# Performance work log

Hardware: AMD Instinct MI355X
Metric: run time of the kernel (lower is better)

Reference implementation:

```python
import jax, jax.numpy as jnp
import numpy as np

N, CIN, T, V, COUT = 64, 64, 256, 25, 128
CI = COUT // 2  # inter_channels
EPS = 1e-5


def setup_inputs() -> dict:
    key = jax.random.key(0)
    ks = jax.random.split(key, 12)
    s = 0.05
    d = {}
    d['x'] = jax.random.normal(ks[0], (N, CIN, T, V), jnp.float32)
    d['A'] = jax.random.normal(ks[1], (3, V, V), jnp.float32) * s
    d['Al'] = jax.random.normal(ks[2], (3, V, V), jnp.float32) * s
    d['Wp'] = jax.random.normal(ks[3], (3, COUT, CIN), jnp.float32) * s
    d['bp'] = jnp.zeros((3, COUT), jnp.float32)
    d['Wm1'] = jax.random.normal(ks[4], (CI, CIN), jnp.float32) * s
    d['bm1'] = jnp.zeros((CI,), jnp.float32)
    d['Wm2'] = jax.random.normal(ks[5], (CI, CIN), jnp.float32) * s
    d['bm2'] = jnp.zeros((CI,), jnp.float32)
    d['Wm3'] = jax.random.normal(ks[6], (COUT, CI), jnp.float32) * s
    d['bm3'] = jnp.zeros((COUT,), jnp.float32)
    d['Wm4'] = jax.random.normal(ks[7], (COUT, CIN), jnp.float32) * s
    d['bm4'] = jnp.zeros((COUT,), jnp.float32)
    d['alpha'] = jax.random.normal(ks[8], (1,), jnp.float32) * s
    d['bn_gamma'] = jnp.ones((COUT,), jnp.float32)
    d['bn_beta'] = jnp.zeros((COUT,), jnp.float32)
    d['down_W'] = jax.random.normal(ks[9], (COUT, CIN), jnp.float32) * s
    d['down_gamma'] = jnp.ones((COUT,), jnp.float32)
    d['down_beta'] = jnp.zeros((COUT,), jnp.float32)
    return d


def _bn_train(y, gamma, beta):
    # BatchNorm2d training forward: biased batch stats over (N, T, V)
    mu = jnp.mean(y, axis=(0, 2, 3), keepdims=True)
    var = jnp.var(y, axis=(0, 2, 3), keepdims=True)
    return (y - mu) * jax.lax.rsqrt(var + EPS) * gamma[None, :, None, None] + beta[None, :, None, None]


def reference(x, A, Al, Wp, bp, Wm1, bm1, Wm2, bm2, Wm3, bm3, Wm4, bm4,
              alpha, bn_gamma, bn_beta, down_W, down_gamma, down_beta):
    Tn = x.shape[2]
    # --- static graph branch: sum over 3 subsets of (A+Al) graph matmuls ---
    Xp = jnp.einsum('soi,nitv->snotv', Wp, x) + bp[:, None, :, None, None]  # (3,N,COUT,T,V)
    y = jnp.einsum('suv,snctv->nctu', A + Al, Xp)                           # (N,COUT,T,V)
    # --- dynamic adjacency from temporal-difference features ---
    xf = jnp.mean(jnp.einsum('oi,nitv->notv', Wm1, x[:, :, :Tn - 2]) + bm1[None, :, None, None], axis=2)  # (N,CI,V)
    xb = jnp.mean(jnp.einsum('oi,nitv->notv', Wm2, x[:, :, 2:]) + bm2[None, :, None, None], axis=2)       # (N,CI,V)
    diff = xb[:, :, :, None] - xf[:, :, None, :]                            # (N,CI,V,V)
    Rd = jnp.tanh(jnp.einsum('oi,nivw->novw', Wm3, diff) + bm3[None, :, None, None])  # (N,COUT,V,V)
    Xm = jnp.einsum('oi,nitv->notv', Wm4, x) + bm4[None, :, None, None]     # (N,COUT,T,V)
    z = jnp.einsum('ncuv,nctv->nctu', Rd, Xm)                               # (N,COUT,T,V)
    y = z * alpha + y
    # --- BN, residual (1x1 conv + BN down-path since CIN != COUT), ReLU ---
    y = _bn_train(y, bn_gamma, bn_beta)
    d = jnp.einsum('oi,nitv->notv', down_W, x)  # no bias
    d = _bn_train(d, down_gamma, down_beta)
    return jax.nn.relu(y + d)
```

## Files before the change

### kernel.cpp

```cpp
#include <hip/hip_runtime.h>
#include <stdint.h>

typedef unsigned short u16;
typedef unsigned int   u32;
typedef short bf16x8 __attribute__((ext_vector_type(8)));
typedef float f32x4  __attribute__((ext_vector_type(4)));

#define N_    64
#define CIN_  64
#define T_    256
#define V_    25
#define COUT_ 128
#define CI_   64
#define EPS_  1e-5f
#define CNT_  409600.0f

#define MFMA16(a,b,c) __builtin_amdgcn_mfma_f32_16x16x32_bf16((a),(b),(c),0,0,0)

__device__ __forceinline__ u16 f2bf(float f) {
  u32 u = __float_as_uint(f);
  u += 0x7fffu + ((u >> 16) & 1u);
  return (u16)(u >> 16);
}
__device__ __forceinline__ float bf2f(u16 h) { return __uint_as_float(((u32)h) << 16); }

__global__ __launch_bounds__(256) void k_pack(const float* __restrict__ Wp, const float* __restrict__ Wm4,
                                              const float* __restrict__ dW, const float* __restrict__ A,
                                              const float* __restrict__ Al,
                                              u16* __restrict__ w5, u16* __restrict__ bst,
                                              float* __restrict__ rsumw) {
  int tid = threadIdx.x;
  for (int i = tid; i < 640 * 64; i += 256) {
    int r = i >> 6, k = i & 63;
    float v = (r < 384) ? Wp[i] : (r < 512) ? Wm4[(r - 384) * 64 + k] : dW[(r - 512) * 64 + k];
    w5[i] = f2bf(v);
  }
  for (int i = tid; i < 3 * 32 * 32; i += 256) {
    int s = i >> 10, rem = i & 1023, u = rem >> 5, v = rem & 31;
    float val = (u < 25 && v < 25) ? (A[(s * 25 + u) * 25 + v] + Al[(s * 25 + u) * 25 + v]) : 0.f;
    bst[i] = f2bf(val);
  }
  if (tid < 75) {
    int s = tid / 25, u = tid % 25;
    float acc = 0.f;
    for (int v = 0; v < 25; v++) acc += A[(s * 25 + u) * 25 + v] + Al[(s * 25 + u) * 25 + v];
    rsumw[tid] = acc;
  }
}

__global__ __launch_bounds__(256) void k_means(const float* __restrict__ x,
                                               float* __restrict__ mf, float* __restrict__ mb) {
  int i = blockIdx.x, n = blockIdx.y;
  const float* src = x + ((size_t)n * CIN_ + i) * T_ * V_;
  __shared__ float xs[T_ * V_];
  __shared__ float pf[8][32], pb[8][32];
  {
    float4* xs4 = (float4*)xs;
    const float4* src4 = (const float4*)src;
    for (int idx = threadIdx.x; idx < (T_ * V_) / 4; idx += 256) xs4[idx] = src4[idx];
  }
  __syncthreads();
  int v = threadIdx.x & 31, g = threadIdx.x >> 5;
  float sf = 0.f, sb = 0.f;
  if (v < V_) {
    for (int t = g; t < T_; t += 8) {
      float val = xs[t * V_ + v];
      if (t < T_ - 2) sf += val;
      if (t >= 2)     sb += val;
    }
  }
  pf[g][v] = sf; pb[g][v] = sb;
  __syncthreads();
  if (threadIdx.x < V_) {
    float af = 0.f, ab = 0.f;
    for (int gg = 0; gg < 8; gg++) { af += pf[gg][threadIdx.x]; ab += pb[gg][threadIdx.x]; }
    size_t o = ((size_t)n * CIN_ + i) * V_ + threadIdx.x;
    mf[o] = af * (1.0f / 254.0f);
    mb[o] = ab * (1.0f / 254.0f);
  }
}

__global__ __launch_bounds__(256) void k_rd1(
    const float* __restrict__ mf, const float* __restrict__ mb,
    const float* __restrict__ Wm1, const float* __restrict__ bm1,
    const float* __restrict__ Wm2, const float* __restrict__ bm2,
    const float* __restrict__ Wm3, float* __restrict__ pqws) {
  int n = blockIdx.x, tid = threadIdx.x;
  __shared__ float MfL[CIN_][V_], MbL[CIN_][V_], xfL[CI_][V_], xbL[CI_][V_];
  for (int idx = tid; idx < CIN_ * V_; idx += 256) {
    MfL[idx / V_][idx % V_] = mf[(size_t)n * CIN_ * V_ + idx];
    MbL[idx / V_][idx % V_] = mb[(size_t)n * CIN_ * V_ + idx];
  }
  __syncthreads();
  for (int idx = tid; idx < CI_ * V_; idx += 256) {
    int o = idx / V_, v = idx % V_;
    float af = bm1[o], ab = bm2[o];
    for (int i = 0; i < CIN_; i++) {
      af += Wm1[o * CIN_ + i] * MfL[i][v];
      ab += Wm2[o * CIN_ + i] * MbL[i][v];
    }
    xfL[o][v] = af; xbL[o][v] = ab;
  }
  __syncthreads();
  for (int idx = tid; idx < COUT_ * V_; idx += 256) {
    int c = idx / V_, u = idx % V_;
    float p = 0.f, q = 0.f;
    for (int i = 0; i < CI_; i++) {
      p += Wm3[c * CI_ + i] * xbL[i][u];
      q += Wm3[c * CI_ + i] * xfL[i][u];
    }
    pqws[(size_t)n * 6400 + idx] = p;
    pqws[(size_t)n * 6400 + 3200 + idx] = q;
  }
}

__global__ __launch_bounds__(256) void k_rd2(
    const float* __restrict__ pqws, const float* __restrict__ rsumw,
    const float* __restrict__ bm3, const float* __restrict__ bm4,
    const float* __restrict__ bp, const float* __restrict__ alpha,
    u16* __restrict__ rdws, float* __restrict__ biasws) {
  int cg = blockIdx.x, n = blockIdx.y;
  int c0 = cg * 16, tid = threadIdx.x;
  __shared__ float Ps[400], Qs[400], rs[75];
  for (int idx = tid; idx < 400; idx += 256) {
    Ps[idx] = pqws[(size_t)n * 6400 + c0 * 25 + idx];
    Qs[idx] = pqws[(size_t)n * 6400 + 3200 + c0 * 25 + idx];
  }
  if (tid < 75) rs[tid] = rsumw[tid];
  __syncthreads();
  float al = alpha[0];
  for (int r = tid; r < 400; r += 256) {
    int cl = r / 25, u = r - cl * 25, c = c0 + cl;
    float pv = Ps[r] + bm3[c];
    float acc = 0.f;
    u16* dst = rdws + ((size_t)(n * COUT_ + c) * 25 + u) * 32;
    for (int w0 = 0; w0 < 25; w0++) {
      float val = al * tanhf(pv - Qs[cl * 25 + w0]);
      dst[w0] = f2bf(val);
      acc += val;
    }
    for (int w0 = 25; w0 < 32; w0++) dst[w0] = 0;
    float yb = 0.f;
    for (int s = 0; s < 3; s++) yb += bp[s * COUT_ + c] * rs[s * 25 + u];
    biasws[(size_t)(n * COUT_ + c) * 25 + u] = bm4[c] * acc + yb;
  }
}

__global__ __launch_bounds__(256, 2) void k_main(
    const float* __restrict__ x, const u16* __restrict__ w5, const u16* __restrict__ bst,
    const u16* __restrict__ rdws, const float* __restrict__ biasws,
    u16* __restrict__ out16, float* __restrict__ partials) {
  __shared__ __align__(16) char smem[36864];
  __shared__ float statsL[512];
  const int tid = threadIdx.x;
  const int w = tid >> 6, l = tid & 63;
  const int lc = l & 15, lq = l >> 4;
  const int n = blockIdx.y, tc = blockIdx.x, t0 = tc * 16;

  bf16x8 bw[3][2];
  #pragma unroll
  for (int s = 0; s < 3; s++)
    #pragma unroll
    for (int ut = 0; ut < 2; ut++)
      bw[s][ut] = *(const bf16x8*)(bst + (s * 32 + ut * 16 + lc) * 32 + lq * 8);

  bf16x8 xf[7][2] = {};
  const float* xb = x + (size_t)n * CIN_ * T_ * V_ + (size_t)t0 * V_;
  #pragma unroll
  for (int ks = 0; ks < 2; ks++) {
    u32* xslw = (u32*)smem;
    for (int idx = tid; idx < 16 * 416; idx += 256) {
      int i2 = idx / 416, p = idx - i2 * 416;
      float a = 0.f, b = 0.f;
      int ch = ks * 32 + 2 * i2;
      if (p < 400) {
        a = xb[(size_t)ch       * (T_ * V_) + p];
        b = xb[(size_t)(ch + 1) * (T_ * V_) + p];
      }
      int f = (p ^ (p >> 2)) & 3;
      xslw[p * 16 + (i2 ^ (f << 2))] = ((u32)f2bf(b) << 16) | (u32)f2bf(a);
    }
    __syncthreads();
    #pragma unroll
    for (int pi = 0; pi < 7; pi++) {
      int pt = w + pi * 4;
      if (pt < 26) {
        int p = pt * 16 + lc;
        int f = (p ^ (p >> 2)) & 3;
        xf[pi][ks] = *(const bf16x8*)((const u16*)smem + p * 32 + ((lq ^ f) << 3));
      }
    }
    __syncthreads();
  }

  {
    uint4 z4 = {0, 0, 0, 0};
    uint4* q = (uint4*)smem;
    for (int idx = tid; idx < 2304; idx += 256) q[idx] = z4;
    statsL[tid] = 0.f; statsL[tid + 256] = 0.f;
  }
  __syncthreads();

  u16* xpl = (u16*)smem;
  const f32x4 zz = {0.f, 0.f, 0.f, 0.f};

  for (int g = 0; g < 8; g++) {
    const int c0 = g * 16;
    f32x4 acc[4][2];
    #pragma unroll
    for (int cl = 0; cl < 4; cl++) { acc[cl][0] = zz; acc[cl][1] = zz; }
    float ds[4] = {0.f, 0.f, 0.f, 0.f}, dq[4] = {0.f, 0.f, 0.f, 0.f};

    #pragma unroll
    for (int h = 0; h < 2; h++) {
      const int nsl = h ? 3 : 2;
      bf16x8 af[3][2];
      #pragma unroll
      for (int si = 0; si < 3; si++) if (si < nsl) {
        int sl = h * 2 + si;
        #pragma unroll
        for (int ks = 0; ks < 2; ks++)
          af[si][ks] = *(const bf16x8*)(w5 + ((sl * 128 + c0 + lc) * 64 + ks * 32 + lq * 8));
      }
      #pragma unroll
      for (int pi = 0; pi < 7; pi++) {
        int pt = w + pi * 4;
        if (pt >= 26) continue;
        f32x4 pa[3];
        #pragma unroll
        for (int si = 0; si < 3; si++) if (si < nsl) {
          pa[si] = MFMA16(af[si][0], xf[pi][0], zz);
          pa[si] = MFMA16(af[si][1], xf[pi][1], pa[si]);
        }
        int p = pt * 16 + lc;
        if (p < 400) {
          u32 up = (u32)p, t = up / 25u, v = up - t * 25u;
          #pragma unroll
          for (int si = 0; si < 3; si++) if (si < nsl) {
            int sl = h * 2 + si;
            if (sl < 4) {
              int slot = sl & 1;
              u16* dst = xpl + (4 * lq) * 1152 + t * 72 + slot * 32 + v;
              #pragma unroll
              for (int r = 0; r < 4; r++) dst[r * 1152] = f2bf(pa[si][r]);
            } else {
              size_t ob = (((size_t)(n * COUT_ + c0 + 4 * lq) * T_ + t0 + t) * V_ + v) * 2 + 1;
              #pragma unroll
              for (int r = 0; r < 4; r++) {
                float dv = pa[si][r];
                out16[ob + (size_t)r * (T_ * V_ * 2)] = f2bf(dv);
                ds[r] += dv; dq[r] += dv * dv;
              }
            }
          }
        }
      }
      if (h == 1) {
        #pragma unroll
        for (int r = 0; r < 4; r++) {
          float a = ds[r], b = dq[r];
          #pragma unroll
          for (int off = 1; off < 16; off <<= 1) { a += __shfl_xor(a, off); b += __shfl_xor(b, off); }
          if (lc == 0) {
            atomicAdd(&statsL[(c0 + 4 * lq + r) * 4 + 2], a);
            atomicAdd(&statsL[(c0 + 4 * lq + r) * 4 + 3], b);
          }
        }
      }
      __syncthreads();

      {
        bf16x8 rdf0[4], rdf1[4];
        if (h == 1) {
          #pragma unroll
          for (int cl = 0; cl < 4; cl++) {
            size_t rb = (size_t)(n * COUT_ + c0 + w * 4 + cl) * 25;
            rdf0[cl] = *(const bf16x8*)(rdws + (rb + lc) * 32 + lq * 8);
            int u1c = (lc + 16 < 25) ? lc + 16 : 24;
            rdf1[cl] = *(const bf16x8*)(rdws + (rb + u1c) * 32 + lq * 8);
          }
        }
        #pragma unroll
        for (int cl = 0; cl < 4; cl++) {
          int clocal = w * 4 + cl;
          #pragma unroll
          for (int kl = 0; kl < 2; kl++) {
            bf16x8 aX = *(const bf16x8*)(xpl + clocal * 1152 + lc * 72 + kl * 32 + lq * 8);
            int kk = h * 2 + kl;
            bf16x8 b0, b1;
            if (kk < 3) { b0 = bw[kk][0]; b1 = bw[kk][1]; }
            else        { b0 = rdf0[cl];  b1 = rdf1[cl]; }
            acc[cl][0] = MFMA16(aX, b0, acc[cl][0]);
            acc[cl][1] = MFMA16(aX, b1, acc[cl][1]);
          }
        }
      }
      if (h == 1) {
        #pragma unroll
        for (int cl = 0; cl < 4; cl++) {
          int c = c0 + w * 4 + cl;
          size_t bb = (size_t)(n * COUT_ + c) * 25;
          float bias0 = biasws[bb + lc];
          int u1 = lc + 16; bool v1 = u1 < 25;
          float bias1 = biasws[bb + (v1 ? u1 : 24)];
          size_t ob = ((size_t)(n * COUT_ + c) * T_ + t0) * V_;
          float sy = 0.f, sq = 0.f;
          #pragma unroll
          for (int r = 0; r < 4; r++) {
            int t = 4 * lq + r;
            float y0 = acc[cl][0][r] + bias0;
            out16[(ob + t * 25 + lc) * 2] = f2bf(y0);
            sy += y0; sq += y0 * y0;
            float y1 = acc[cl][1][r] + bias1;
            if (v1) {
              out16[(ob + t * 25 + u1) * 2] = f2bf(y1);
              sy += y1; sq += y1 * y1;
            }
          }
          #pragma unroll
          for (int off = 1; off < 64; off <<= 1) { sy += __shfl_xor(sy, off); sq += __shfl_xor(sq, off); }
          if (l == 0) { atomicAdd(&statsL[c * 4 + 0], sy); atomicAdd(&statsL[c * 4 + 1], sq); }
        }
      }
      __syncthreads();
    }
  }
  int bflat = blockIdx.y * 16 + blockIdx.x;
  for (int j = tid; j < 512; j += 256) partials[(size_t)j * 1024 + bflat] = statsL[j];
}

__global__ __launch_bounds__(256) void k_stats1(const float* __restrict__ partials, float* __restrict__ colsum) {
  int w = threadIdx.x >> 6, l = threadIdx.x & 63;
  for (int ci = 0; ci < 8; ci++) {
    int j = blockIdx.x * 32 + w * 8 + ci;
    float s = 0.f;
    for (int it = 0; it < 16; it++) s += partials[(size_t)j * 1024 + it * 64 + l];
    #pragma unroll
    for (int off = 1; off < 64; off <<= 1) s += __shfl_xor(s, off);
    if (l == 0) colsum[j] = s;
  }
}

__global__ __launch_bounds__(128) void k_stats2(
    const float* __restrict__ colsum,
    const float* __restrict__ bn_g, const float* __restrict__ bn_b,
    const float* __restrict__ dn_g, const float* __restrict__ dn_b,
    float* __restrict__ params) {
  int c = threadIdx.x;
  float sy = colsum[c * 4], syy = colsum[c * 4 + 1], sd = colsum[c * 4 + 2], sdd = colsum[c * 4 + 3];
  float muY = sy / CNT_, varY = syy / CNT_ - muY * muY;
  float muD = sd / CNT_, varD = sdd / CNT_ - muD * muD;
  float sY = bn_g[c] * rsqrtf(varY + EPS_);
  float sD = dn_g[c] * rsqrtf(varD + EPS_);
  float off = bn_b[c] - muY * sY + dn_b[c] - muD * sD;
  params[c * 4 + 0] = sY; params[c * 4 + 1] = sD; params[c * 4 + 2] = off;
}

__global__ __launch_bounds__(256) void k_final(u32* __restrict__ io, const float* __restrict__ params) {
  int slab = blockIdx.x;
  int c = slab & (COUT_ - 1);
  float sY = params[c * 4], sD = params[c * 4 + 1], off = params[c * 4 + 2];
  uint4* io4 = (uint4*)io + (size_t)slab * 1600;
  #pragma unroll
  for (int j = 0; j < 7; j++) {
    int idx = j * 256 + (int)threadIdx.x;
    if (idx < 1600) {
      uint4 wv = io4[idx];
      uint4 o;
      o.x = __float_as_uint(fmaxf(fmaf(bf2f((u16)(wv.x & 0xffffu)), sY, fmaf(bf2f((u16)(wv.x >> 16)), sD, off)), 0.f));
      o.y = __float_as_uint(fmaxf(fmaf(bf2f((u16)(wv.y & 0xffffu)), sY, fmaf(bf2f((u16)(wv.y >> 16)), sD, off)), 0.f));
      o.z = __float_as_uint(fmaxf(fmaf(bf2f((u16)(wv.z & 0xffffu)), sY, fmaf(bf2f((u16)(wv.z >> 16)), sD, off)), 0.f));
      o.w = __float_as_uint(fmaxf(fmaf(bf2f((u16)(wv.w & 0xffffu)), sY, fmaf(bf2f((u16)(wv.w >> 16)), sD, off)), 0.f));
      io4[idx] = o;
    }
  }
}

extern "C" void kernel_launch(void* const* d_in, const int* in_sizes, int n_in,
                              void* d_out, int out_size, void* d_ws, size_t ws_size,
                              hipStream_t stream) {
  const float* x    = (const float*)d_in[0];
  const float* A    = (const float*)d_in[1];
  const float* Al   = (const float*)d_in[2];
  const float* Wp   = (const float*)d_in[3];
  const float* bp   = (const float*)d_in[4];
  const float* Wm1  = (const float*)d_in[5];
  const float* bm1  = (const float*)d_in[6];
  const float* Wm2  = (const float*)d_in[7];
  const float* bm2  = (const float*)d_in[8];
  const float* Wm3  = (const float*)d_in[9];
  const float* bm3  = (const float*)d_in[10];
  const float* Wm4  = (const float*)d_in[11];
  const float* bm4  = (const float*)d_in[12];
  const float* alpha= (const float*)d_in[13];
  const float* bn_g = (const float*)d_in[14];
  const float* bn_b = (const float*)d_in[15];
  const float* dW   = (const float*)d_in[16];
  const float* dn_g = (const float*)d_in[17];
  const float* dn_b = (const float*)d_in[18];

  char* ws = (char*)d_ws;
  float* mf       = (float*)(ws + 0);
  float* mb       = (float*)(ws + 409600);
  u16*   rdws     = (u16*)  (ws + 819200);
  float* biasws   = (float*)(ws + 13926400);
  u16*   w5       = (u16*)  (ws + 14745600);
  u16*   bstw     = (u16*)  (ws + 14827520);
  float* partials = (float*)(ws + 14833664);
  float* colsum   = (float*)(ws + 16930816);
  float* params   = (float*)(ws + 16932864);
  float* pqws  = partials;
  float* rsumw = colsum;

  k_pack <<<dim3(1),       dim3(256), 0, stream>>>(Wp, Wm4, dW, A, Al, w5, bstw, rsumw);
  k_means<<<dim3(64, 64),  dim3(256), 0, stream>>>(x, mf, mb);
  k_rd1  <<<dim3(64),      dim3(256), 0, stream>>>(mf, mb, Wm1, bm1, Wm2, bm2, Wm3, pqws);
  k_rd2  <<<dim3(8, 64),   dim3(256), 0, stream>>>(pqws, rsumw, bm3, bm4, bp, alpha, rdws, biasws);
  k_main <<<dim3(16, 64),  dim3(256), 0, stream>>>(x, w5, bstw, rdws, biasws,
                                                   (u16*)d_out, partials);
  k_stats1<<<dim3(16),     dim3(256), 0, stream>>>(partials, colsum);
  k_stats2<<<dim3(1),      dim3(128), 0, stream>>>(colsum, bn_g, bn_b, dn_g, dn_b, params);
  k_final<<<dim3(64 * 128),dim3(256), 0, stream>>>((u32*)d_out, params);
}
```

Before: 666.7 us.

## Double k_main block to 512 threads and stage down-path in LDS for packed stores

k_main now runs 8 waves per block, so each wave handles half as many pixel tiles and output channels. The down-path conv results are no longer written straight to global memory as strided 16-bit values. They are staged in a new LDS buffer and later combined with the main output into single 32-bit packed stores, with their BN statistics computed in the same reduction pass. This removes the scattered half-word global writes and one set of shuffle reductions, at the cost of more LDS, lower per-thread register reuse, and down-path stats computed from bf16-rounded values.

```diff
diff --git a/kernel.cpp b/kernel.cpp
--- a/kernel.cpp
+++ b/kernel.cpp
@@ -146,11 +146,12 @@
   }
 }
 
-__global__ __launch_bounds__(256, 2) void k_main(
+__global__ __launch_bounds__(512, 4) void k_main(
     const float* __restrict__ x, const u16* __restrict__ w5, const u16* __restrict__ bst,
     const u16* __restrict__ rdws, const float* __restrict__ biasws,
     u16* __restrict__ out16, float* __restrict__ partials) {
   __shared__ __align__(16) char smem[36864];
+  __shared__ u16 dls[16 * 408];
   __shared__ float statsL[512];
   const int tid = threadIdx.x;
   const int w = tid >> 6, l = tid & 63;
@@ -164,12 +165,12 @@
     for (int ut = 0; ut < 2; ut++)
       bw[s][ut] = *(const bf16x8*)(bst + (s * 32 + ut * 16 + lc) * 32 + lq * 8);
 
-  bf16x8 xf[7][2] = {};
+  bf16x8 xf[4][2] = {};
   const float* xb = x + (size_t)n * CIN_ * T_ * V_ + (size_t)t0 * V_;
   #pragma unroll
   for (int ks = 0; ks < 2; ks++) {
     u32* xslw = (u32*)smem;
-    for (int idx = tid; idx < 16 * 416; idx += 256) {
+    for (int idx = tid; idx < 16 * 416; idx += 512) {
       int i2 = idx / 416, p = idx - i2 * 416;
       float a = 0.f, b = 0.f;
       int ch = ks * 32 + 2 * i2;
@@ -182,8 +183,8 @@
     }
     __syncthreads();
     #pragma unroll
-    for (int pi = 0; pi < 7; pi++) {
-      int pt = w + pi * 4;
+    for (int pi = 0; pi < 4; pi++) {
+      int pt = w + pi * 8;
       if (pt < 26) {
         int p = pt * 16 + lc;
         int f = (p ^ (p >> 2)) & 3;
@@ -196,20 +197,20 @@
   {
     uint4 z4 = {0, 0, 0, 0};
     uint4* q = (uint4*)smem;
-    for (int idx = tid; idx < 2304; idx += 256) q[idx] = z4;
-    statsL[tid] = 0.f; statsL[tid + 256] = 0.f;
+    for (int idx = tid; idx < 2304; idx += 512) q[idx] = z4;
+    statsL[tid] = 0.f;
   }
   __syncthreads();
 
   u16* xpl = (u16*)smem;
   const f32x4 zz = {0.f, 0.f, 0.f, 0.f};
+  u32* out32 = (u32*)out16;
 
   for (int g = 0; g < 8; g++) {
     const int c0 = g * 16;
-    f32x4 acc[4][2];
+    f32x4 acc[2][2];
     #pragma unroll
-    for (int cl = 0; cl < 4; cl++) { acc[cl][0] = zz; acc[cl][1] = zz; }
-    float ds[4] = {0.f, 0.f, 0.f, 0.f}, dq[4] = {0.f, 0.f, 0.f, 0.f};
+    for (int cl = 0; cl < 2; cl++) { acc[cl][0] = zz; acc[cl][1] = zz; }
 
     #pragma unroll
     for (int h = 0; h < 2; h++) {
@@ -223,66 +224,46 @@
           af[si][ks] = *(const bf16x8*)(w5 + ((sl * 128 + c0 + lc) * 64 + ks * 32 + lq * 8));
       }
       #pragma unroll
-      for (int pi = 0; pi < 7; pi++) {
-        int pt = w + pi * 4;
-        if (pt >= 26) continue;
-        f32x4 pa[3];
+      for (int si = 0; si < 3; si++) if (si < nsl) {
+        int sl = h * 2 + si;
         #pragma unroll
-        for (int si = 0; si < 3; si++) if (si < nsl) {
-          pa[si] = MFMA16(af[si][0], xf[pi][0], zz);
-          pa[si] = MFMA16(af[si][1], xf[pi][1], pa[si]);
-        }
-        int p = pt * 16 + lc;
-        if (p < 400) {
-          u32 up = (u32)p, t = up / 25u, v = up - t * 25u;
-          #pragma unroll
-          for (int si = 0; si < 3; si++) if (si < nsl) {
-            int sl = h * 2 + si;
+        for (int pi = 0; pi < 4; pi++) {
+          int pt = w + pi * 8;
+          if (pt >= 26) continue;
+          f32x4 pa = MFMA16(af[si][0], xf[pi][0], zz);
+          pa = MFMA16(af[si][1], xf[pi][1], pa);
+          int p = pt * 16 + lc;
+          if (p < 400) {
+            u32 up = (u32)p, t = up / 25u, v = up - t * 25u;
             if (sl < 4) {
               int slot = sl & 1;
               u16* dst = xpl + (4 * lq) * 1152 + t * 72 + slot * 32 + v;
               #pragma unroll
-              for (int r = 0; r < 4; r++) dst[r * 1152] = f2bf(pa[si][r]);
+              for (int r = 0; r < 4; r++) dst[r * 1152] = f2bf(pa[r]);
             } else {
-              size_t ob = (((size_t)(n * COUT_ + c0 + 4 * lq) * T_ + t0 + t) * V_ + v) * 2 + 1;
+              u16* dd = dls + (4 * lq) * 408 + p;
               #pragma unroll
-              for (int r = 0; r < 4; r++) {
-                float dv = pa[si][r];
-                out16[ob + (size_t)r * (T_ * V_ * 2)] = f2bf(dv);
-                ds[r] += dv; dq[r] += dv * dv;
-              }
+              for (int r = 0; r < 4; r++) dd[r * 408] = f2bf(pa[r]);
             }
           }
         }
       }
-      if (h == 1) {
-        #pragma unroll
-        for (int r = 0; r < 4; r++) {
-          float a = ds[r], b = dq[r];
-          #pragma unroll
-          for (int off = 1; off < 16; off <<= 1) { a += __shfl_xor(a, off); b += __shfl_xor(b, off); }
-          if (lc == 0) {
-            atomicAdd(&statsL[(c0 + 4 * lq + r) * 4 + 2], a);
-            atomicAdd(&statsL[(c0 + 4 * lq + r) * 4 + 3], b);
-          }
-        }
-      }
       __syncthreads();
 
       {
-        bf16x8 rdf0[4], rdf1[4];
+        bf16x8 rdf0[2], rdf1[2];
         if (h == 1) {
           #pragma unroll
-          for (int cl = 0; cl < 4; cl++) {
-            size_t rb = (size_t)(n * COUT_ + c0 + w * 4 + cl) * 25;
+          for (int cl = 0; cl < 2; cl++) {
+            size_t rb = (size_t)(n * COUT_ + c0 + w * 2 + cl) * 25;
             rdf0[cl] = *(const bf16x8*)(rdws + (rb + lc) * 32 + lq * 8);
             int u1c = (lc + 16 < 25) ? lc + 16 : 24;
             rdf1[cl] = *(const bf16x8*)(rdws + (rb + u1c) * 32 + lq * 8);
           }
         }
         #pragma unroll
-        for (int cl = 0; cl < 4; cl++) {
-          int clocal = w * 4 + cl;
+        for (int cl = 0; cl < 2; cl++) {
+          int clocal = w * 2 + cl;
           #pragma unroll
           for (int kl = 0; kl < 2; kl++) {
             bf16x8 aX = *(const bf16x8*)(xpl + clocal * 1152 + lc * 72 + kl * 32 + lq * 8);
@@ -297,36 +278,47 @@
       }
       if (h == 1) {
         #pragma unroll
-        for (int cl = 0; cl < 4; cl++) {
-          int c = c0 + w * 4 + cl;
+        for (int cl = 0; cl < 2; cl++) {
+          int c = c0 + w * 2 + cl;
           size_t bb = (size_t)(n * COUT_ + c) * 25;
           float bias0 = biasws[bb + lc];
           int u1 = lc + 16; bool v1 = u1 < 25;
           float bias1 = biasws[bb + (v1 ? u1 : 24)];
           size_t ob = ((size_t)(n * COUT_ + c) * T_ + t0) * V_;
-          float sy = 0.f, sq = 0.f;
+          const u16* dd = dls + (w * 2 + cl) * 408;
+          float sy = 0.f, sq = 0.f, sd = 0.f, sdd = 0.f;
           #pragma unroll
           for (int r = 0; r < 4; r++) {
             int t = 4 * lq + r;
             float y0 = acc[cl][0][r] + bias0;
-            out16[(ob + t * 25 + lc) * 2] = f2bf(y0);
+            u16 d0 = dd[t * 25 + lc];
+            out32[ob + t * 25 + lc] = ((u32)d0 << 16) | (u32)f2bf(y0);
             sy += y0; sq += y0 * y0;
-            float y1 = acc[cl][1][r] + bias1;
+            float f0 = bf2f(d0); sd += f0; sdd += f0 * f0;
             if (v1) {
-              out16[(ob + t * 25 + u1) * 2] = f2bf(y1);
+              float y1 = acc[cl][1][r] + bias1;
+              u16 d1 = dd[t * 25 + u1];
+              out32[ob + t * 25 + u1] = ((u32)d1 << 16) | (u32)f2bf(y1);
               sy += y1; sq += y1 * y1;
+              float f1 = bf2f(d1); sd += f1; sdd += f1 * f1;
             }
           }
           #pragma unroll
-          for (int off = 1; off < 64; off <<= 1) { sy += __shfl_xor(sy, off); sq += __shfl_xor(sq, off); }
-          if (l == 0) { atomicAdd(&statsL[c * 4 + 0], sy); atomicAdd(&statsL[c * 4 + 1], sq); }
+          for (int off = 1; off < 64; off <<= 1) {
+            sy += __shfl_xor(sy, off); sq += __shfl_xor(sq, off);
+            sd += __shfl_xor(sd, off); sdd += __shfl_xor(sdd, off);
+          }
+          if (l == 0) {
+            atomicAdd(&statsL[c * 4 + 0], sy); atomicAdd(&statsL[c * 4 + 1], sq);
+            atomicAdd(&statsL[c * 4 + 2], sd); atomicAdd(&statsL[c * 4 + 3], sdd);
+          }
         }
       }
       __syncthreads();
     }
   }
   int bflat = blockIdx.y * 16 + blockIdx.x;
-  for (int j = tid; j < 512; j += 256) partials[(size_t)j * 1024 + bflat] = statsL[j];
+  for (int j = tid; j < 512; j += 512) partials[(size_t)j * 1024 + bflat] = statsL[j];
 }
 
 __global__ __launch_bounds__(256) void k_stats1(const float* __restrict__ partials, float* __restrict__ colsum) {
@@ -416,7 +408,7 @@
   k_means<<<dim3(64, 64),  dim3(256), 0, stream>>>(x, mf, mb);
   k_rd1  <<<dim3(64),      dim3(256), 0, stream>>>(mf, mb, Wm1, bm1, Wm2, bm2, Wm3, pqws);
   k_rd2  <<<dim3(8, 64),   dim3(256), 0, stream>>>(pqws, rsumw, bm3, bm4, bp, alpha, rdws, biasws);
-  k_main <<<dim3(16, 64),  dim3(256), 0, stream>>>(x, w5, bstw, rdws, biasws,
+  k_main <<<dim3(16, 64),  dim3(512), 0, stream>>>(x, w5, bstw, rdws, biasws,
                                                    (u16*)d_out, partials);
   k_stats1<<<dim3(16),     dim3(256), 0, stream>>>(partials, colsum);
   k_stats2<<<dim3(1),      dim3(128), 0, stream>>>(colsum, bn_g, bn_b, dn_g, dn_b, params);
```

Measured after the change: 673.3 us. Within noise of the previous version (+1.0%).
